# Performance work log

Hardware: AMD Instinct MI355X
Metric: run time of the kernel (lower is better)

## Reference

```python
import jax, jax.numpy as jnp
import numpy as np

COLOR_SIZE = 8
FILTERS = 64
LAYERS = 4
CUMSUM_NORM = 256 * 256 * 3  # hardcoded in original: /256/256/3


def setup_inputs() -> dict:
    key = jax.random.key(0)
    k0, k1, k2, k3 = jax.random.split(key, 4)
    s = 0.05
    example = jax.random.randint(k0, (4, 256, 256, 3), 0, COLOR_SIZE, dtype=jnp.int32)
    # per-channel Dense stacks: layer 0 has input dim 1, layers 1..3 have input dim FILTERS
    W_in_first = jax.random.normal(k1, (3, 1, FILTERS), dtype=jnp.float32) * s
    b_in_first = jnp.zeros((3, FILTERS), dtype=jnp.float32)
    W_in_rest = jax.random.normal(k2, (LAYERS - 1, 3, FILTERS, FILTERS), dtype=jnp.float32) * s
    b_in_rest = jnp.zeros((LAYERS - 1, 3, FILTERS), dtype=jnp.float32)
    W_final = jax.random.normal(k3, (3, FILTERS, COLOR_SIZE), dtype=jnp.float32) * s
    b_final = jnp.zeros((3, COLOR_SIZE), dtype=jnp.float32)
    return {
        "example": example,
        "W_in_first": W_in_first, "b_in_first": b_in_first,
        "W_in_rest": W_in_rest, "b_in_rest": b_in_rest,
        "W_final": W_final, "b_final": b_final,
    }


def reference(example, W_in_first, b_in_first, W_in_rest, b_in_rest, W_final, b_final):
    # example: [B, H, W, 3] int in [0, COLOR_SIZE)
    x = example.astype(jnp.float32) / COLOR_SIZE * 2.0 - 1.0
    B, H, W, _ = x.shape
    L = H * W
    x = x.reshape(B, L, 3, 1)

    def layer(x, Wl, bl):
        # per-channel dense + relu: [B, L, 3, din] x [3, din, dout] -> [B, L, 3, dout]
        x = jax.nn.relu(jnp.einsum('blcd,cde->blce', x, Wl) + bl)
        # flatten channels into the sequence and take causal running sum
        x = x.reshape(B, L * 3, FILTERS)
        x = jnp.cumsum(x, axis=-2) / CUMSUM_NORM
        return x.reshape(B, L, 3, FILTERS)

    x = layer(x, W_in_first, b_in_first)
    for i in range(LAYERS - 1):
        x = layer(x, W_in_rest[i], b_in_rest[i])

    # final per-channel dense to color logits (no activation)
    x = jnp.einsum('blcd,cde->blce', x, W_final) + b_final
    return x.reshape(B, H, W, 3, COLOR_SIZE)
```

## Files before the change

kernel.cpp:

```cpp
#include <hip/hip_runtime.h>
#include <stdint.h>


#define BB 4
#define SP 65536
#define SS 196608
#define CI 1024
#define NG 16
#define INVN (1.0f / 196608.0f)

typedef __attribute__((ext_vector_type(8))) _Float16 half8;
typedef __attribute__((ext_vector_type(4))) float    f32x4;

__global__ __launch_bounds__(256)
void prep(const int* __restrict__ ex, const float* __restrict__ W0,
          const float* __restrict__ b0, const float* __restrict__ Wr,
          const float* __restrict__ Wfin,
          _Float16* __restrict__ Wt16, _Float16* __restrict__ Wf16p,
          float* __restrict__ Wf32, float* __restrict__ tab32,
          int* __restrict__ Hsub, int* __restrict__ Hgrp)
{
    __shared__ int hist[64][24];
    int tid = threadIdx.x, bi = blockIdx.x;
    int b = bi >> 4, g = bi & 15;
    for (int i = tid; i < 1536; i += 256) hist[i / 24][i % 24] = 0;
    __syncthreads();
    for (int q = 0; q < 16; ++q) {
        int pl = q * 256 + tid;
        const int* ep = ex + ((size_t)b * SP + g * 4096 + pl) * 3;
        int j = pl >> 6;
        atomicAdd(&hist[j][ep[0]], 1);
        atomicAdd(&hist[j][8 + ep[1]], 1);
        atomicAdd(&hist[j][16 + ep[2]], 1);
    }
    __syncthreads();
    for (int i = tid; i < 1536; i += 256) {
        int j = i / 24, cv = i % 24;
        Hsub[(size_t)(b * CI + g * 64 + j) * 24 + cv] = hist[j][cv];
    }
    if (tid < 24) {
        int s = 0;
        for (int j = 0; j < 64; ++j) s += hist[j][tid];
        Hgrp[(size_t)(b * NG + g) * 24 + tid] = s;
    }
    {
        int i0 = bi * 256 + tid, nth = 64 * 256;
        for (int idx = i0; idx < 36864; idx += nth) {
            int d = idx & 63, f = (idx >> 6) & 63, lc = idx >> 12;
            Wt16[idx] = (_Float16)Wr[(size_t)(lc * 64 + d) * 64 + f];
        }
        for (int idx = i0; idx < 3072; idx += nth) {
            int d = idx & 63, n = (idx >> 6) & 15, c = idx >> 10;
            Wf16p[idx] = (n < 8) ? (_Float16)Wfin[(size_t)(c * 64 + d) * 8 + n]
                                 : (_Float16)0.f;
        }
        for (int idx = i0; idx < 1536; idx += nth) {
            int d = idx & 63, ck = idx >> 6;
            Wf32[idx] = Wfin[(size_t)((ck >> 3) * 64 + d) * 8 + (ck & 7)];
        }
        for (int idx = i0; idx < 1536; idx += nth) {
            int f = idx & 63, v = (idx >> 6) & 7, c = idx >> 9;
            float xv = v * 0.25f - 1.0f;
            tab32[idx] = fmaxf(W0[c * 64 + f] * xv + b0[c * 64 + f], 0.f);
        }
    }
}

__global__ __launch_bounds__(256, 4)
void midA(const int* __restrict__ ex,
          const int* __restrict__ Hsub, const int* __restrict__ Hgrp,
          const float* __restrict__ tab32,
          const _Float16* __restrict__ W16, const float* __restrict__ Wd32,
          const float* __restrict__ bias, _Float16* __restrict__ Y,
          float* __restrict__ A64, float* __restrict__ Ggrp)
{
    __shared__ float stab[1536];
    __shared__ __align__(16) _Float16 bounce3[3][64 * 72];
    __shared__ float segwt[3][4][64];
    __shared__ float basearr[192];
    __shared__ float hpart[4][24];
    __shared__ float carry[64];

    int tid = threadIdx.x, bi = blockIdx.x;
    int b = bi >> 10, ci = bi & 1023, g = ci >> 6, cr = ci & 63;
    int w = tid >> 6, ln = tid & 63, lm = ln & 15, lq = ln >> 4;
    int P0 = ci * 64;

    for (int i = tid; i < 1536; i += 256) stab[i] = tab32[i];
    if (ln < 24) {
        float s = 0.f;
        for (int j = w; j < g; j += 4)
            s += (float)Hgrp[(size_t)(b * NG + j) * 24 + ln];
        const int* hp = Hsub + (size_t)(b * CI + g * 64) * 24 + ln;
        for (int j = w; j < cr; j += 4) s += (float)hp[j * 24];
        hpart[w][ln] = s;
    }
    __syncthreads();

    float y0[3][16];
    {
#pragma unroll
        for (int p = 0; p < 16; ++p) {
            const int* ep = ex + ((size_t)b * SP + P0 + w * 16 + p) * 3;
            y0[0][p] = stab[ep[0] * 64 + ln];
            y0[1][p] = stab[(8 + ep[1]) * 64 + ln];
            y0[2][p] = stab[(16 + ep[2]) * 64 + ln];
        }
#pragma unroll
        for (int c = 0; c < 3; ++c)
#pragma unroll
            for (int p = 1; p < 16; ++p) y0[c][p] += y0[c][p - 1];
#pragma unroll
        for (int c = 0; c < 3; ++c) segwt[c][w][ln] = y0[c][15];
    }
    if (tid < 64) {
        float c0 = 0.f;
#pragma unroll
        for (int cv = 0; cv < 24; ++cv) {
            float cnt = hpart[0][cv] + hpart[1][cv] + hpart[2][cv] + hpart[3][cv];
            c0 += cnt * stab[cv * 64 + tid];
        }
        carry[tid] = c0;
    }
    __syncthreads();

    {
        float off0[3];
#pragma unroll
        for (int c = 0; c < 3; ++c) {
            float o = 0.f;
            for (int w2 = 0; w2 < w; ++w2) o += segwt[c][w2][ln];
            off0[c] = o;
        }
#pragma unroll
        for (int p = 0; p < 16; ++p) {
            float S0 = y0[0][p] + off0[0], S1 = y0[1][p] + off0[1], S2 = y0[2][p] + off0[2];
            float P1 = p ? y0[1][p - 1] + off0[1] : off0[1];
            float P2 = p ? y0[2][p - 1] + off0[2] : off0[2];
            int row = w * 16 + p;
            bounce3[0][row * 72 + ln] = (_Float16)(S0 + P1 + P2);
            bounce3[1][row * 72 + ln] = (_Float16)(S0 + S1 + P2);
            bounce3[2][row * 72 + ln] = (_Float16)(S0 + S1 + S2);
        }
    }
    if (tid < 192) {
        int c = tid >> 6, f = tid & 63;
        const float* wp = Wd32 + (size_t)(c * 64) * 64 + f;
        float a = 0.f;
        for (int d = 0; d < 64; ++d) a += carry[d] * wp[d * 64];
        basearr[tid] = bias[tid] + INVN * a;
    }
    __syncthreads();

    f32x4 acc[3][4];
#pragma unroll
    for (int c = 0; c < 3; ++c) {
        const half8* bb = (const half8*)&bounce3[c][0];
        half8 a0 = bb[(w * 16 + lm) * 9 + lq];
        half8 a1 = bb[(w * 16 + lm) * 9 + 4 + lq];
#pragma unroll
        for (int nt = 0; nt < 4; ++nt) {
            const half8* bp = (const half8*)(W16 + (size_t)(c * 64 + nt * 16 + lm) * 64);
            f32x4 t = {0.f, 0.f, 0.f, 0.f};
            t = __builtin_amdgcn_mfma_f32_16x16x32_f16(a0, bp[lq],     t, 0, 0, 0);
            t = __builtin_amdgcn_mfma_f32_16x16x32_f16(a1, bp[4 + lq], t, 0, 0, 0);
            acc[c][nt] = t;
        }
    }

    float s[3][4][4], wexcl[3][4];
#pragma unroll
    for (int c = 0; c < 3; ++c)
#pragma unroll
        for (int nt = 0; nt < 4; ++nt) {
            float base = basearr[c * 64 + nt * 16 + lm];
            float run = 0.f;
#pragma unroll
            for (int r = 0; r < 4; ++r) {
                float yv = fmaxf(base + INVN * acc[c][nt][r], 0.f);
                run += yv; s[c][nt][r] = run;
            }
            float v = run;
            float t1 = __shfl_up(v, 16); if (lq >= 1) v += t1;
            float t2 = __shfl_up(v, 32); if (lq >= 2) v += t2;
            wexcl[c][nt] = v - run;
            if (lq == 3) segwt[c][w][nt * 16 + lm] = v;
        }
    __syncthreads();

    {
        float off[3][4], tot[3][4];
#pragma unroll
        for (int c = 0; c < 3; ++c)
#pragma unroll
            for (int nt = 0; nt < 4; ++nt) {
                float o = wexcl[c][nt], ts = 0.f;
#pragma unroll
                for (int w2 = 0; w2 < 4; ++w2) {
                    float wv = segwt[c][w2][nt * 16 + lm];
                    ts += wv;
                    if (w2 < w) o += wv;
                }
                off[c][nt] = o; tot[c][nt] = ts;
            }
        if (w == 0 && lq == 0)
#pragma unroll
            for (int nt = 0; nt < 4; ++nt) {
                float t3 = tot[0][nt] + tot[1][nt] + tot[2][nt];
                A64[(size_t)(b * CI + ci) * 64 + nt * 16 + lm] = t3;
                atomicAdd(&Ggrp[(size_t)(b * NG + g) * 64 + nt * 16 + lm], t3);
            }
#pragma unroll
        for (int nt = 0; nt < 4; ++nt)
#pragma unroll
            for (int r = 0; r < 4; ++r) {
                float S0 = off[0][nt] + s[0][nt][r];
                float S1 = off[1][nt] + s[1][nt][r];
                float S2 = off[2][nt] + s[2][nt][r];
                float P1 = off[1][nt] + (r ? s[1][nt][r - 1] : 0.f);
                float P2 = off[2][nt] + (r ? s[2][nt][r - 1] : 0.f);
                int row = w * 16 + lq * 4 + r;
                bounce3[0][row * 72 + nt * 16 + lm] = (_Float16)(S0 + P1 + P2);
                bounce3[1][row * 72 + nt * 16 + lm] = (_Float16)(S0 + S1 + P2);
                bounce3[2][row * 72 + nt * 16 + lm] = (_Float16)(S0 + S1 + S2);
            }
    }
    __syncthreads();
#pragma unroll
    for (int q = 0; q < 6; ++q) {
        int idx = q * 256 + tid;
        int c = idx >> 9, rem = idx & 511;
        int pix = rem >> 3, f8 = rem & 7;
        half8 v = *(const half8*)&bounce3[c][pix * 72 + f8 * 8];
        ((half8*)(Y + ((size_t)(b * 3 + c) * SP + P0 + pix) * 64))[f8] = v;
    }
}

__global__ __launch_bounds__(256, 4)
void midB(const _Float16* Yin, _Float16* Yout,
          const float* __restrict__ A64p, const float* __restrict__ Ggrp_p,
          const _Float16* __restrict__ W16, const float* __restrict__ Wd32,
          const float* __restrict__ bias,
          float* __restrict__ A64, float* __restrict__ Ggrp)
{
    __shared__ __align__(16) _Float16 bounce3[3][64 * 72];
    __shared__ float wtop[3][4][64];
    __shared__ float basearr[192];
    __shared__ float cpart[4][64];
    __shared__ float carry[64];

    int tid = threadIdx.x, bi = blockIdx.x;
    int b = bi >> 10, ci = bi & 1023, g = ci >> 6, cr = ci & 63;
    int w = tid >> 6, ln = tid & 63, lm = ln & 15, lq = ln >> 4;
    int P0 = ci * 64;

    half8 af0[3], af1[3];
#pragma unroll
    for (int c = 0; c < 3; ++c) {
        const half8* ap = (const half8*)(Yin + ((size_t)(b * 3 + c) * SP + P0 + w * 16 + lm) * 64);
        af0[c] = ap[lq]; af1[c] = ap[4 + lq];
    }
    {
        float s = 0.f;
        for (int j = w; j < g; j += 4)
            s += Ggrp_p[(size_t)(b * NG + j) * 64 + ln];
        const float* ap = A64p + (size_t)(b * CI + g * 64) * 64 + ln;
        for (int j = w; j < cr; j += 4) s += ap[j * 64];
        cpart[w][ln] = s;
    }
    __syncthreads();
    if (tid < 64)
        carry[tid] = cpart[0][tid] + cpart[1][tid] + cpart[2][tid] + cpart[3][tid];
    __syncthreads();
    if (tid < 192) {
        int c = tid >> 6, f = tid & 63;
        const float* wp = Wd32 + (size_t)(c * 64) * 64 + f;
        float a = 0.f;
        for (int d = 0; d < 64; ++d) a += carry[d] * wp[d * 64];
        basearr[tid] = bias[tid] + INVN * a;
    }
    __syncthreads();

    f32x4 acc[3][4];
#pragma unroll
    for (int c = 0; c < 3; ++c)
#pragma unroll
        for (int nt = 0; nt < 4; ++nt) {
            const half8* bp = (const half8*)(W16 + (size_t)(c * 64 + nt * 16 + lm) * 64);
            f32x4 t = {0.f, 0.f, 0.f, 0.f};
            t = __builtin_amdgcn_mfma_f32_16x16x32_f16(af0[c], bp[lq],     t, 0, 0, 0);
            t = __builtin_amdgcn_mfma_f32_16x16x32_f16(af1[c], bp[4 + lq], t, 0, 0, 0);
            acc[c][nt] = t;
        }

    float s[3][4][4], wexcl[3][4];
#pragma unroll
    for (int c = 0; c < 3; ++c)
#pragma unroll
        for (int nt = 0; nt < 4; ++nt) {
            float base = basearr[c * 64 + nt * 16 + lm];
            float run = 0.f;
#pragma unroll
            for (int r = 0; r < 4; ++r) {
                float yv = fmaxf(base + INVN * acc[c][nt][r], 0.f);
                run += yv; s[c][nt][r] = run;
            }
            float v = run;
            float t1 = __shfl_up(v, 16); if (lq >= 1) v += t1;
            float t2 = __shfl_up(v, 32); if (lq >= 2) v += t2;
            wexcl[c][nt] = v - run;
            if (lq == 3) wtop[c][w][nt * 16 + lm] = v;
        }
    __syncthreads();

    {
        float off[3][4], tot[3][4];
#pragma unroll
        for (int c = 0; c < 3; ++c)
#pragma unroll
            for (int nt = 0; nt < 4; ++nt) {
                float o = wexcl[c][nt], ts = 0.f;
#pragma unroll
                for (int w2 = 0; w2 < 4; ++w2) {
                    float wv = wtop[c][w2][nt * 16 + lm];
                    ts += wv;
                    if (w2 < w) o += wv;
                }
                off[c][nt] = o; tot[c][nt] = ts;
            }
        if (w == 0 && lq == 0)
#pragma unroll
            for (int nt = 0; nt < 4; ++nt) {
                float t3 = tot[0][nt] + tot[1][nt] + tot[2][nt];
                A64[(size_t)(b * CI + ci) * 64 + nt * 16 + lm] = t3;
                atomicAdd(&Ggrp[(size_t)(b * NG + g) * 64 + nt * 16 + lm], t3);
            }
#pragma unroll
        for (int nt = 0; nt < 4; ++nt)
#pragma unroll
            for (int r = 0; r < 4; ++r) {
                float S0 = off[0][nt] + s[0][nt][r];
                float S1 = off[1][nt] + s[1][nt][r];
                float S2 = off[2][nt] + s[2][nt][r];
                float P1 = off[1][nt] + (r ? s[1][nt][r - 1] : 0.f);
                float P2 = off[2][nt] + (r ? s[2][nt][r - 1] : 0.f);
                int row = w * 16 + lq * 4 + r;
                bounce3[0][row * 72 + nt * 16 + lm] = (_Float16)(S0 + P1 + P2);
                bounce3[1][row * 72 + nt * 16 + lm] = (_Float16)(S0 + S1 + P2);
                bounce3[2][row * 72 + nt * 16 + lm] = (_Float16)(S0 + S1 + S2);
            }
    }
    __syncthreads();
#pragma unroll
    for (int q = 0; q < 6; ++q) {
        int idx = q * 256 + tid;
        int c = idx >> 9, rem = idx & 511;
        int pix = rem >> 3, f8 = rem & 7;
        half8 v = *(const half8*)&bounce3[c][pix * 72 + f8 * 8];
        ((half8*)(Yout + ((size_t)(b * 3 + c) * SP + P0 + pix) * 64))[f8] = v;
    }
}

__global__ __launch_bounds__(256, 4)
void midC(const _Float16* __restrict__ Yin,
          const float* __restrict__ A64p, const float* __restrict__ Ggrp_p,
          const _Float16* __restrict__ W16, const float* __restrict__ Wd32,
          const float* __restrict__ bias,
          const _Float16* __restrict__ Wf16p, const float* __restrict__ bfin,
          float* __restrict__ out, float* __restrict__ A64, float* __restrict__ Ggrp)
{
    __shared__ __align__(16) _Float16 bounce3[3][64 * 72];
    __shared__ float wtop[3][4][64];
    __shared__ float basearr[192];
    __shared__ float cpart[4][64];
    __shared__ float carry[64];
    __shared__ __align__(16) float outst[64 * 28];

    int tid = threadIdx.x, bi = blockIdx.x;
    int b = bi >> 10, ci = bi & 1023, g = ci >> 6, cr = ci & 63;
    int w = tid >> 6, ln = tid & 63, lm = ln & 15, lq = ln >> 4;
    int P0 = ci * 64;

    half8 af0[3], af1[3];
#pragma unroll
    for (int c = 0; c < 3; ++c) {
        const half8* ap = (const half8*)(Yin + ((size_t)(b * 3 + c) * SP + P0 + w * 16 + lm) * 64);
        af0[c] = ap[lq]; af1[c] = ap[4 + lq];
    }
    {
        float s = 0.f;
        for (int j = w; j < g; j += 4)
            s += Ggrp_p[(size_t)(b * NG + j) * 64 + ln];
        const float* ap = A64p + (size_t)(b * CI + g * 64) * 64 + ln;
        for (int j = w; j < cr; j += 4) s += ap[j * 64];
        cpart[w][ln] = s;
    }
    __syncthreads();
    if (tid < 64)
        carry[tid] = cpart[0][tid] + cpart[1][tid] + cpart[2][tid] + cpart[3][tid];
    __syncthreads();
    if (tid < 192) {
        int c = tid >> 6, f = tid & 63;
        const float* wp = Wd32 + (size_t)(c * 64) * 64 + f;
        float a = 0.f;
        for (int d = 0; d < 64; ++d) a += carry[d] * wp[d * 64];
        basearr[tid] = bias[tid] + INVN * a;
    }
    __syncthreads();

    f32x4 acc[3][4];
#pragma unroll
    for (int c = 0; c < 3; ++c)
#pragma unroll
        for (int nt = 0; nt < 4; ++nt) {
            const half8* bp = (const half8*)(W16 + (size_t)(c * 64 + nt * 16 + lm) * 64);
            f32x4 t = {0.f, 0.f, 0.f, 0.f};
            t = __builtin_amdgcn_mfma_f32_16x16x32_f16(af0[c], bp[lq],     t, 0, 0, 0);
            t = __builtin_amdgcn_mfma_f32_16x16x32_f16(af1[c], bp[4 + lq], t, 0, 0, 0);
            acc[c][nt] = t;
        }

    float s[3][4][4], wexcl[3][4];
#pragma unroll
    for (int c = 0; c < 3; ++c)
#pragma unroll
        for (int nt = 0; nt < 4; ++nt) {
            float base = basearr[c * 64 + nt * 16 + lm];
            float run = 0.f;
#pragma unroll
            for (int r = 0; r < 4; ++r) {
                float yv = fmaxf(base + INVN * acc[c][nt][r], 0.f);
                run += yv; s[c][nt][r] = run;
            }
            float v = run;
            float t1 = __shfl_up(v, 16); if (lq >= 1) v += t1;
            float t2 = __shfl_up(v, 32); if (lq >= 2) v += t2;
            wexcl[c][nt] = v - run;
            if (lq == 3) wtop[c][w][nt * 16 + lm] = v;
        }
    __syncthreads();

    {
        float off[3][4], tot[3][4];
#pragma unroll
        for (int c = 0; c < 3; ++c)
#pragma unroll
            for (int nt = 0; nt < 4; ++nt) {
                float o = wexcl[c][nt], ts = 0.f;
#pragma unroll
                for (int w2 = 0; w2 < 4; ++w2) {
                    float wv = wtop[c][w2][nt * 16 + lm];
                    ts += wv;
                    if (w2 < w) o += wv;
                }
                off[c][nt] = o; tot[c][nt] = ts;
            }
        if (w == 0 && lq == 0)
#pragma unroll
            for (int nt = 0; nt < 4; ++nt) {
                float t3 = tot[0][nt] + tot[1][nt] + tot[2][nt];
                A64[(size_t)(b * CI + ci) * 64 + nt * 16 + lm] = t3;
                atomicAdd(&Ggrp[(size_t)(b * NG + g) * 64 + nt * 16 + lm], t3);
            }
#pragma unroll
        for (int nt = 0; nt < 4; ++nt)
#pragma unroll
            for (int r = 0; r < 4; ++r) {
                float S0 = off[0][nt] + s[0][nt][r];
                float S1 = off[1][nt] + s[1][nt][r];
                float S2 = off[2][nt] + s[2][nt][r];
                float P1 = off[1][nt] + (r ? s[1][nt][r - 1] : 0.f);
                float P2 = off[2][nt] + (r ? s[2][nt][r - 1] : 0.f);
                int row = w * 16 + lq * 4 + r;
                bounce3[0][row * 72 + nt * 16 + lm] = (_Float16)(S0 + P1 + P2);
                bounce3[1][row * 72 + nt * 16 + lm] = (_Float16)(S0 + S1 + P2);
                bounce3[2][row * 72 + nt * 16 + lm] = (_Float16)(S0 + S1 + S2);
            }
    }
    __syncthreads();

#pragma unroll
    for (int c = 0; c < 3; ++c) {
        const half8* bb = (const half8*)&bounce3[c][0];
        half8 fa0 = bb[(w * 16 + lm) * 9 + lq];
        half8 fa1 = bb[(w * 16 + lm) * 9 + 4 + lq];
        const half8* fb = (const half8*)(Wf16p + (size_t)(c * 16 + lm) * 64);
        f32x4 t = {0.f, 0.f, 0.f, 0.f};
        t = __builtin_amdgcn_mfma_f32_16x16x32_f16(fa0, fb[lq],     t, 0, 0, 0);
        t = __builtin_amdgcn_mfma_f32_16x16x32_f16(fa1, fb[4 + lq], t, 0, 0, 0);
        if (lm < 8) {
            float bz = bfin[c * 8 + lm];
#pragma unroll
            for (int r = 0; r < 4; ++r)
                outst[(w * 16 + lq * 4 + r) * 28 + c * 8 + lm] = bz + INVN * t[r];
        }
    }
    __syncthreads();
    {
        float4* obase = (float4*)(out + ((size_t)b * SS + (size_t)P0 * 3) * 8);
#pragma unroll
        for (int k = 0; k < 2; ++k) {
            int idx = k * 256 + tid;
            if (idx < 384) {
                int pix = idx / 6, sub = (idx % 6) * 4;
                obase[idx] = *(const float4*)&outst[pix * 28 + sub];
            }
        }
    }
}

__global__ __launch_bounds__(256, 4)
void fixk(const float* __restrict__ A64p, const float* __restrict__ Ggrp_p,
          const float* __restrict__ Wf32, float* __restrict__ out)
{
    __shared__ float cpart[4][64];
    __shared__ float carry[64];
    __shared__ float vfix[24];
    int tid = threadIdx.x, bi = blockIdx.x;
    int b = bi >> 10, ci = bi & 1023, g = ci >> 6, cr = ci & 63;
    int w = tid >> 6, ln = tid & 63;
    int P0 = ci * 64;

    {
        float s = 0.f;
        for (int j = w; j < g; j += 4)
            s += Ggrp_p[(size_t)(b * NG + j) * 64 + ln];
        const float* ap = A64p + (size_t)(b * CI + g * 64) * 64 + ln;
        for (int j = w; j < cr; j += 4) s += ap[j * 64];
        cpart[w][ln] = s;
    }
    __syncthreads();
    if (tid < 64)
        carry[tid] = cpart[0][tid] + cpart[1][tid] + cpart[2][tid] + cpart[3][tid];
    __syncthreads();
    if (tid < 24) {
        float vf = 0.f;
        for (int d = 0; d < 64; ++d) vf += carry[d] * Wf32[tid * 64 + d];
        vfix[tid] = INVN * vf;
    }
    __syncthreads();
    float4* obase = (float4*)(out + ((size_t)b * SS + (size_t)P0 * 3) * 8);
#pragma unroll
    for (int k = 0; k < 2; ++k) {
        int idx = k * 256 + tid;
        if (idx < 384) {
            int sub = (idx % 6) * 4;
            float4 v = obase[idx];
            v.x += vfix[sub];
            v.y += vfix[sub + 1];
            v.z += vfix[sub + 2];
            v.w += vfix[sub + 3];
            obase[idx] = v;
        }
    }
}

extern "C" void kernel_launch(void* const* d_in, const int* in_sizes, int n_in,
                              void* d_out, int out_size, void* d_ws, size_t ws_size,
                              hipStream_t stream)
{
    const int*   ex   = (const int*)d_in[0];
    const float* W0   = (const float*)d_in[1];
    const float* b0   = (const float*)d_in[2];
    const float* Wr   = (const float*)d_in[3];
    const float* br   = (const float*)d_in[4];
    const float* Wfin = (const float*)d_in[5];
    const float* bfin = (const float*)d_in[6];
    float* out = (float*)d_out;

    char* ws = (char*)d_ws;
    size_t off = 0;
    _Float16* Y = (_Float16*)(ws + off); off += (size_t)BB * 3 * SP * 64 * 2;
    float* Ggrp1 = (float*)(ws + off); off += (size_t)BB * NG * 64 * 4;
    float* Ggrp2 = (float*)(ws + off); off += (size_t)BB * NG * 64 * 4;
    float* Ggrp3 = (float*)(ws + off); off += (size_t)BB * NG * 64 * 4;
    float* A64_1 = (float*)(ws + off); off += (size_t)BB * CI * 64 * 4;
    float* A64_2 = (float*)(ws + off); off += (size_t)BB * CI * 64 * 4;
    float* A64_3 = (float*)(ws + off); off += (size_t)BB * CI * 64 * 4;
    int* Hsub = (int*)(ws + off); off += (size_t)BB * CI * 24 * 4;
    int* Hgrp = (int*)(ws + off); off += (size_t)BB * NG * 24 * 4;
    _Float16* Wt16  = (_Float16*)(ws + off); off += 36864 * 2;
    _Float16* Wf16p = (_Float16*)(ws + off); off += 3072 * 2;
    float* Wf32  = (float*)(ws + off); off += 1536 * 4;
    float* tab32 = (float*)(ws + off); off += 1536 * 4;

    hipMemsetAsync(Ggrp1, 0, 3 * (size_t)BB * NG * 64 * 4, stream);
    prep<<<64, 256, 0, stream>>>(ex, W0, b0, Wr, Wfin,
                                 Wt16, Wf16p, Wf32, tab32, Hsub, Hgrp);
    midA<<<4096, 256, 0, stream>>>(ex, Hsub, Hgrp, tab32,
                                   Wt16, Wr, br, Y, A64_1, Ggrp1);
    midB<<<4096, 256, 0, stream>>>(Y, Y, A64_1, Ggrp1,
                                   Wt16 + 12288, Wr + 12288, br + 192,
                                   A64_2, Ggrp2);
    midC<<<4096, 256, 0, stream>>>(Y, A64_2, Ggrp2,
                                   Wt16 + 24576, Wr + 24576, br + 384,
                                   Wf16p, bfin, out, A64_3, Ggrp3);
    fixk<<<4096, 256, 0, stream>>>(A64_3, Ggrp3, Wf32, out);
}
```

Baseline: 365.2 us.

## Shrink LDS staging buffers, raise occupancy, widen prep grid, parallelize fix reduction

```diff
diff --git a/kernel.cpp b/kernel.cpp
--- a/kernel.cpp
+++ b/kernel.cpp
@@ -20,31 +20,31 @@
           float* __restrict__ Wf32, float* __restrict__ tab32,
           int* __restrict__ Hsub, int* __restrict__ Hgrp)
 {
-    __shared__ int hist[64][24];
+    __shared__ int hist[16][24];
     int tid = threadIdx.x, bi = blockIdx.x;
-    int b = bi >> 4, g = bi & 15;
-    for (int i = tid; i < 1536; i += 256) hist[i / 24][i % 24] = 0;
-    __syncthreads();
-    for (int q = 0; q < 16; ++q) {
-        int pl = q * 256 + tid;
-        const int* ep = ex + ((size_t)b * SP + g * 4096 + pl) * 3;
+    int b = bi >> 6, g = (bi >> 2) & 15, q = bi & 3;
+    for (int i = tid; i < 384; i += 256) hist[i / 24][i % 24] = 0;
+    __syncthreads();
+    for (int it = 0; it < 4; ++it) {
+        int pl = it * 256 + tid;
+        const int* ep = ex + ((size_t)b * SP + g * 4096 + q * 1024 + pl) * 3;
         int j = pl >> 6;
         atomicAdd(&hist[j][ep[0]], 1);
         atomicAdd(&hist[j][8 + ep[1]], 1);
         atomicAdd(&hist[j][16 + ep[2]], 1);
     }
     __syncthreads();
-    for (int i = tid; i < 1536; i += 256) {
+    for (int i = tid; i < 384; i += 256) {
         int j = i / 24, cv = i % 24;
-        Hsub[(size_t)(b * CI + g * 64 + j) * 24 + cv] = hist[j][cv];
+        Hsub[(size_t)(b * CI + g * 64 + q * 16 + j) * 24 + cv] = hist[j][cv];
     }
     if (tid < 24) {
         int s = 0;
-        for (int j = 0; j < 64; ++j) s += hist[j][tid];
-        Hgrp[(size_t)(b * NG + g) * 24 + tid] = s;
-    }
-    {
-        int i0 = bi * 256 + tid, nth = 64 * 256;
+        for (int j = 0; j < 16; ++j) s += hist[j][tid];
+        atomicAdd(&Hgrp[(size_t)(b * NG + g) * 24 + tid], s);
+    }
+    {
+        int i0 = bi * 256 + tid, nth = 256 * 256;
         for (int idx = i0; idx < 36864; idx += nth) {
             int d = idx & 63, f = (idx >> 6) & 63, lc = idx >> 12;
             Wt16[idx] = (_Float16)Wr[(size_t)(lc * 64 + d) * 64 + f];
@@ -66,7 +66,7 @@
     }
 }
 
-__global__ __launch_bounds__(256, 4)
+__global__ __launch_bounds__(256, 6)
 void midA(const int* __restrict__ ex,
           const int* __restrict__ Hsub, const int* __restrict__ Hgrp,
           const float* __restrict__ tab32,
@@ -75,7 +75,7 @@
           float* __restrict__ A64, float* __restrict__ Ggrp)
 {
     __shared__ float stab[1536];
-    __shared__ __align__(16) _Float16 bounce3[3][64 * 72];
+    __shared__ __align__(16) _Float16 bounce[64 * 72];
     __shared__ float segwt[3][4][64];
     __shared__ float basearr[192];
     __shared__ float hpart[4][24];
@@ -124,24 +124,12 @@
     }
     __syncthreads();
 
-    {
-        float off0[3];
-#pragma unroll
-        for (int c = 0; c < 3; ++c) {
-            float o = 0.f;
-            for (int w2 = 0; w2 < w; ++w2) o += segwt[c][w2][ln];
-            off0[c] = o;
-        }
-#pragma unroll
-        for (int p = 0; p < 16; ++p) {
-            float S0 = y0[0][p] + off0[0], S1 = y0[1][p] + off0[1], S2 = y0[2][p] + off0[2];
-            float P1 = p ? y0[1][p - 1] + off0[1] : off0[1];
-            float P2 = p ? y0[2][p - 1] + off0[2] : off0[2];
-            int row = w * 16 + p;
-            bounce3[0][row * 72 + ln] = (_Float16)(S0 + P1 + P2);
-            bounce3[1][row * 72 + ln] = (_Float16)(S0 + S1 + P2);
-            bounce3[2][row * 72 + ln] = (_Float16)(S0 + S1 + S2);
-        }
+    float off0[3];
+#pragma unroll
+    for (int c = 0; c < 3; ++c) {
+        float o = 0.f;
+        for (int w2 = 0; w2 < w; ++w2) o += segwt[c][w2][ln];
+        off0[c] = o;
     }
     if (tid < 192) {
         int c = tid >> 6, f = tid & 63;
@@ -150,23 +138,35 @@
         for (int d = 0; d < 64; ++d) a += carry[d] * wp[d * 64];
         basearr[tid] = bias[tid] + INVN * a;
     }
-    __syncthreads();
+
+    half8 af0[3], af1[3];
+#pragma unroll
+    for (int c = 0; c < 3; ++c) {
+#pragma unroll
+        for (int p = 0; p < 16; ++p) {
+            float a0 = y0[0][p] + off0[0];
+            float a1 = (c >= 1 ? y0[1][p] : (p ? y0[1][p - 1] : 0.f)) + off0[1];
+            float a2 = (c == 2 ? y0[2][p] : (p ? y0[2][p - 1] : 0.f)) + off0[2];
+            bounce[(w * 16 + p) * 72 + ln] = (_Float16)(a0 + a1 + a2);
+        }
+        __syncthreads();
+        const half8* bb = (const half8*)bounce;
+        af0[c] = bb[(w * 16 + lm) * 9 + lq];
+        af1[c] = bb[(w * 16 + lm) * 9 + 4 + lq];
+        __syncthreads();
+    }
 
     f32x4 acc[3][4];
 #pragma unroll
-    for (int c = 0; c < 3; ++c) {
-        const half8* bb = (const half8*)&bounce3[c][0];
-        half8 a0 = bb[(w * 16 + lm) * 9 + lq];
-        half8 a1 = bb[(w * 16 + lm) * 9 + 4 + lq];
+    for (int c = 0; c < 3; ++c)
 #pragma unroll
         for (int nt = 0; nt < 4; ++nt) {
             const half8* bp = (const half8*)(W16 + (size_t)(c * 64 + nt * 16 + lm) * 64);
             f32x4 t = {0.f, 0.f, 0.f, 0.f};
-            t = __builtin_amdgcn_mfma_f32_16x16x32_f16(a0, bp[lq],     t, 0, 0, 0);
-            t = __builtin_amdgcn_mfma_f32_16x16x32_f16(a1, bp[4 + lq], t, 0, 0, 0);
+            t = __builtin_amdgcn_mfma_f32_16x16x32_f16(af0[c], bp[lq],     t, 0, 0, 0);
+            t = __builtin_amdgcn_mfma_f32_16x16x32_f16(af1[c], bp[4 + lq], t, 0, 0, 0);
             acc[c][nt] = t;
         }
-    }
 
     float s[3][4][4], wexcl[3][4];
 #pragma unroll
@@ -210,40 +210,33 @@
                 A64[(size_t)(b * CI + ci) * 64 + nt * 16 + lm] = t3;
                 atomicAdd(&Ggrp[(size_t)(b * NG + g) * 64 + nt * 16 + lm], t3);
             }
-#pragma unroll
-        for (int nt = 0; nt < 4; ++nt)
+        _Float16* Y0 = Y + ((size_t)(b * 3) * SP + P0 + w * 16 + lq * 4) * 64 + lm;
+        _Float16* Y1 = Y0 + (size_t)SP * 64;
+        _Float16* Y2 = Y1 + (size_t)SP * 64;
+#pragma unroll
+        for (int nt = 0; nt < 4; ++nt) {
+            float offT = off[0][nt] + off[1][nt] + off[2][nt];
 #pragma unroll
             for (int r = 0; r < 4; ++r) {
-                float S0 = off[0][nt] + s[0][nt][r];
-                float S1 = off[1][nt] + s[1][nt][r];
-                float S2 = off[2][nt] + s[2][nt][r];
-                float P1 = off[1][nt] + (r ? s[1][nt][r - 1] : 0.f);
-                float P2 = off[2][nt] + (r ? s[2][nt][r - 1] : 0.f);
-                int row = w * 16 + lq * 4 + r;
-                bounce3[0][row * 72 + nt * 16 + lm] = (_Float16)(S0 + P1 + P2);
-                bounce3[1][row * 72 + nt * 16 + lm] = (_Float16)(S0 + S1 + P2);
-                bounce3[2][row * 72 + nt * 16 + lm] = (_Float16)(S0 + S1 + S2);
-            }
-    }
-    __syncthreads();
-#pragma unroll
-    for (int q = 0; q < 6; ++q) {
-        int idx = q * 256 + tid;
-        int c = idx >> 9, rem = idx & 511;
-        int pix = rem >> 3, f8 = rem & 7;
-        half8 v = *(const half8*)&bounce3[c][pix * 72 + f8 * 8];
-        ((half8*)(Y + ((size_t)(b * 3 + c) * SP + P0 + pix) * 64))[f8] = v;
+                float s1p = r ? s[1][nt][r - 1] : 0.f;
+                float s2p = r ? s[2][nt][r - 1] : 0.f;
+                float V  = offT + s[0][nt][r];
+                float Wv = V + s[1][nt][r];
+                Y0[r * 64 + nt * 16] = (_Float16)(V + s1p + s2p);
+                Y1[r * 64 + nt * 16] = (_Float16)(Wv + s2p);
+                Y2[r * 64 + nt * 16] = (_Float16)(Wv + s[2][nt][r]);
+            }
+        }
     }
 }
 
-__global__ __launch_bounds__(256, 4)
+__global__ __launch_bounds__(256, 8)
 void midB(const _Float16* Yin, _Float16* Yout,
           const float* __restrict__ A64p, const float* __restrict__ Ggrp_p,
           const _Float16* __restrict__ W16, const float* __restrict__ Wd32,
           const float* __restrict__ bias,
           float* __restrict__ A64, float* __restrict__ Ggrp)
 {
-    __shared__ __align__(16) _Float16 bounce3[3][64 * 72];
     __shared__ float wtop[3][4][64];
     __shared__ float basearr[192];
     __shared__ float cpart[4][64];
@@ -268,6 +261,18 @@
         for (int j = w; j < cr; j += 4) s += ap[j * 64];
         cpart[w][ln] = s;
     }
+
+    f32x4 acc[3][4];
+#pragma unroll
+    for (int c = 0; c < 3; ++c)
+#pragma unroll
+        for (int nt = 0; nt < 4; ++nt) {
+            const half8* bp = (const half8*)(W16 + (size_t)(c * 64 + nt * 16 + lm) * 64);
+            f32x4 t = {0.f, 0.f, 0.f, 0.f};
+            t = __builtin_amdgcn_mfma_f32_16x16x32_f16(af0[c], bp[lq],     t, 0, 0, 0);
+            t = __builtin_amdgcn_mfma_f32_16x16x32_f16(af1[c], bp[4 + lq], t, 0, 0, 0);
+            acc[c][nt] = t;
+        }
     __syncthreads();
     if (tid < 64)
         carry[tid] = cpart[0][tid] + cpart[1][tid] + cpart[2][tid] + cpart[3][tid];
@@ -281,18 +286,6 @@
     }
     __syncthreads();
 
-    f32x4 acc[3][4];
-#pragma unroll
-    for (int c = 0; c < 3; ++c)
-#pragma unroll
-        for (int nt = 0; nt < 4; ++nt) {
-            const half8* bp = (const half8*)(W16 + (size_t)(c * 64 + nt * 16 + lm) * 64);
-            f32x4 t = {0.f, 0.f, 0.f, 0.f};
-            t = __builtin_amdgcn_mfma_f32_16x16x32_f16(af0[c], bp[lq],     t, 0, 0, 0);
-            t = __builtin_amdgcn_mfma_f32_16x16x32_f16(af1[c], bp[4 + lq], t, 0, 0, 0);
-            acc[c][nt] = t;
-        }
-
     float s[3][4][4], wexcl[3][4];
 #pragma unroll
     for (int c = 0; c < 3; ++c)
@@ -335,33 +328,27 @@
                 A64[(size_t)(b * CI + ci) * 64 + nt * 16 + lm] = t3;
                 atomicAdd(&Ggrp[(size_t)(b * NG + g) * 64 + nt * 16 + lm], t3);
             }
-#pragma unroll
-        for (int nt = 0; nt < 4; ++nt)
+        _Float16* Y0 = Yout + ((size_t)(b * 3) * SP + P0 + w * 16 + lq * 4) * 64 + lm;
+        _Float16* Y1 = Y0 + (size_t)SP * 64;
+        _Float16* Y2 = Y1 + (size_t)SP * 64;
+#pragma unroll
+        for (int nt = 0; nt < 4; ++nt) {
+            float offT = off[0][nt] + off[1][nt] + off[2][nt];
 #pragma unroll
             for (int r = 0; r < 4; ++r) {
-                float S0 = off[0][nt] + s[0][nt][r];
-                float S1 = off[1][nt] + s[1][nt][r];
-                float S2 = off[2][nt] + s[2][nt][r];
-                float P1 = off[1][nt] + (r ? s[1][nt][r - 1] : 0.f);
-                float P2 = off[2][nt] + (r ? s[2][nt][r - 1] : 0.f);
-                int row = w * 16 + lq * 4 + r;
-                bounce3[0][row * 72 + nt * 16 + lm] = (_Float16)(S0 + P1 + P2);
-                bounce3[1][row * 72 + nt * 16 + lm] = (_Float16)(S0 + S1 + P2);
-                bounce3[2][row * 72 + nt * 16 + lm] = (_Float16)(S0 + S1 + S2);
-            }
-    }
-    __syncthreads();
-#pragma unroll
-    for (int q = 0; q < 6; ++q) {
-        int idx = q * 256 + tid;
-        int c = idx >> 9, rem = idx & 511;
-        int pix = rem >> 3, f8 = rem & 7;
-        half8 v = *(const half8*)&bounce3[c][pix * 72 + f8 * 8];
-        ((half8*)(Yout + ((size_t)(b * 3 + c) * SP + P0 + pix) * 64))[f8] = v;
+                float s1p = r ? s[1][nt][r - 1] : 0.f;
+                float s2p = r ? s[2][nt][r - 1] : 0.f;
+                float V  = offT + s[0][nt][r];
+                float Wv = V + s[1][nt][r];
+                Y0[r * 64 + nt * 16] = (_Float16)(V + s1p + s2p);
+                Y1[r * 64 + nt * 16] = (_Float16)(Wv + s2p);
+                Y2[r * 64 + nt * 16] = (_Float16)(Wv + s[2][nt][r]);
+            }
+        }
     }
 }
 
-__global__ __launch_bounds__(256, 4)
+__global__ __launch_bounds__(256, 6)
 void midC(const _Float16* __restrict__ Yin,
           const float* __restrict__ A64p, const float* __restrict__ Ggrp_p,
           const _Float16* __restrict__ W16, const float* __restrict__ Wd32,
@@ -369,12 +356,11 @@
           const _Float16* __restrict__ Wf16p, const float* __restrict__ bfin,
           float* __restrict__ out, float* __restrict__ A64, float* __restrict__ Ggrp)
 {
-    __shared__ __align__(16) _Float16 bounce3[3][64 * 72];
+    __shared__ __align__(16) _Float16 bounce[64 * 72];
     __shared__ float wtop[3][4][64];
     __shared__ float basearr[192];
     __shared__ float cpart[4][64];
     __shared__ float carry[64];
-    __shared__ __align__(16) float outst[64 * 28];
 
     int tid = threadIdx.x, bi = blockIdx.x;
     int b = bi >> 10, ci = bi & 1023, g = ci >> 6, cr = ci & 63;
@@ -395,6 +381,18 @@
         for (int j = w; j < cr; j += 4) s += ap[j * 64];
         cpart[w][ln] = s;
     }
+
+    f32x4 acc[3][4];
+#pragma unroll
+    for (int c = 0; c < 3; ++c)
+#pragma unroll
+        for (int nt = 0; nt < 4; ++nt) {
+            const half8* bp = (const half8*)(W16 + (size_t)(c * 64 + nt * 16 + lm) * 64);
+            f32x4 t = {0.f, 0.f, 0.f, 0.f};
+            t = __builtin_amdgcn_mfma_f32_16x16x32_f16(af0[c], bp[lq],     t, 0, 0, 0);
+            t = __builtin_amdgcn_mfma_f32_16x16x32_f16(af1[c], bp[4 + lq], t, 0, 0, 0);
+            acc[c][nt] = t;
+        }
     __syncthreads();
     if (tid < 64)
         carry[tid] = cpart[0][tid] + cpart[1][tid] + cpart[2][tid] + cpart[3][tid];
@@ -408,18 +406,6 @@
     }
     __syncthreads();
 
-    f32x4 acc[3][4];
-#pragma unroll
-    for (int c = 0; c < 3; ++c)
-#pragma unroll
-        for (int nt = 0; nt < 4; ++nt) {
-            const half8* bp = (const half8*)(W16 + (size_t)(c * 64 + nt * 16 + lm) * 64);
-            f32x4 t = {0.f, 0.f, 0.f, 0.f};
-            t = __builtin_amdgcn_mfma_f32_16x16x32_f16(af0[c], bp[lq],     t, 0, 0, 0);
-            t = __builtin_amdgcn_mfma_f32_16x16x32_f16(af1[c], bp[4 + lq], t, 0, 0, 0);
-            acc[c][nt] = t;
-        }
-
     float s[3][4][4], wexcl[3][4];
 #pragma unroll
     for (int c = 0; c < 3; ++c)
@@ -440,8 +426,9 @@
         }
     __syncthreads();
 
-    {
-        float off[3][4], tot[3][4];
+    float off[3][4];
+    {
+        float tot[3][4];
 #pragma unroll
         for (int c = 0; c < 3; ++c)
 #pragma unroll
@@ -462,26 +449,27 @@
                 A64[(size_t)(b * CI + ci) * 64 + nt * 16 + lm] = t3;
                 atomicAdd(&Ggrp[(size_t)(b * NG + g) * 64 + nt * 16 + lm], t3);
             }
-#pragma unroll
-        for (int nt = 0; nt < 4; ++nt)
+    }
+
+#pragma unroll
+    for (int c = 0; c < 3; ++c) {
+#pragma unroll
+        for (int nt = 0; nt < 4; ++nt) {
+            float offT = off[0][nt] + off[1][nt] + off[2][nt];
 #pragma unroll
             for (int r = 0; r < 4; ++r) {
-                float S0 = off[0][nt] + s[0][nt][r];
-                float S1 = off[1][nt] + s[1][nt][r];
-                float S2 = off[2][nt] + s[2][nt][r];
-                float P1 = off[1][nt] + (r ? s[1][nt][r - 1] : 0.f);
-                float P2 = off[2][nt] + (r ? s[2][nt][r - 1] : 0.f);
-                int row = w * 16 + lq * 4 + r;
-                bounce3[0][row * 72 + nt * 16 + lm] = (_Float16)(S0 + P1 + P2);
-                bounce3[1][row * 72 + nt * 16 + lm] = (_Float16)(S0 + S1 + P2);
-                bounce3[2][row * 72 + nt * 16 + lm] = (_Float16)(S0 + S1 + S2);
-            }
-    }
-    __syncthreads();
-
-#pragma unroll
-    for (int c = 0; c < 3; ++c) {
-        const half8* bb = (const half8*)&bounce3[c][0];
+                float s1p = r ? s[1][nt][r - 1] : 0.f;
+                float s2p = r ? s[2][nt][r - 1] : 0.f;
+                float V = offT + s[0][nt][r];
+                float ov;
+                if (c == 0)      ov = V + s1p + s2p;
+                else if (c == 1) ov = V + s[1][nt][r] + s2p;
+                else             ov = V + s[1][nt][r] + s[2][nt][r];
+                bounce[(w * 16 + lq * 4 + r) * 72 + nt * 16 + lm] = (_Float16)ov;
+            }
+        }
+        __syncthreads();
+        const half8* bb = (const half8*)bounce;
         half8 fa0 = bb[(w * 16 + lm) * 9 + lq];
         half8 fa1 = bb[(w * 16 + lm) * 9 + 4 + lq];
         const half8* fb = (const half8*)(Wf16p + (size_t)(c * 16 + lm) * 64);
@@ -490,31 +478,22 @@
         t = __builtin_amdgcn_mfma_f32_16x16x32_f16(fa1, fb[4 + lq], t, 0, 0, 0);
         if (lm < 8) {
             float bz = bfin[c * 8 + lm];
+            float* ob = out + ((size_t)b * SS + (size_t)(P0 + w * 16 + lq * 4) * 3 + c) * 8 + lm;
 #pragma unroll
             for (int r = 0; r < 4; ++r)
-                outst[(w * 16 + lq * 4 + r) * 28 + c * 8 + lm] = bz + INVN * t[r];
-        }
-    }
-    __syncthreads();
-    {
-        float4* obase = (float4*)(out + ((size_t)b * SS + (size_t)P0 * 3) * 8);
-#pragma unroll
-        for (int k = 0; k < 2; ++k) {
-            int idx = k * 256 + tid;
-            if (idx < 384) {
-                int pix = idx / 6, sub = (idx % 6) * 4;
-                obase[idx] = *(const float4*)&outst[pix * 28 + sub];
-            }
-        }
+                ob[r * 24] = bz + INVN * t[r];
+        }
+        __syncthreads();
     }
 }
 
-__global__ __launch_bounds__(256, 4)
+__global__ __launch_bounds__(256, 8)
 void fixk(const float* __restrict__ A64p, const float* __restrict__ Ggrp_p,
           const float* __restrict__ Wf32, float* __restrict__ out)
 {
     __shared__ float cpart[4][64];
     __shared__ float carry[64];
+    __shared__ float part[24][8];
     __shared__ float vfix[24];
     int tid = threadIdx.x, bi = blockIdx.x;
     int b = bi >> 10, ci = bi & 1023, g = ci >> 6, cr = ci & 63;
@@ -533,9 +512,20 @@
     if (tid < 64)
         carry[tid] = cpart[0][tid] + cpart[1][tid] + cpart[2][tid] + cpart[3][tid];
     __syncthreads();
+    if (tid < 192) {
+        int ck = tid >> 3, sg = tid & 7;
+        const float* wp = Wf32 + ck * 64 + sg * 8;
+        const float* cp = carry + sg * 8;
+        float vf = 0.f;
+#pragma unroll
+        for (int d = 0; d < 8; ++d) vf += cp[d] * wp[d];
+        part[ck][sg] = vf;
+    }
+    __syncthreads();
     if (tid < 24) {
         float vf = 0.f;
-        for (int d = 0; d < 64; ++d) vf += carry[d] * Wf32[tid * 64 + d];
+#pragma unroll
+        for (int j = 0; j < 8; ++j) vf += part[tid][j];
         vfix[tid] = INVN * vf;
     }
     __syncthreads();
@@ -585,8 +575,9 @@
     float* tab32 = (float*)(ws + off); off += 1536 * 4;
 
     hipMemsetAsync(Ggrp1, 0, 3 * (size_t)BB * NG * 64 * 4, stream);
-    prep<<<64, 256, 0, stream>>>(ex, W0, b0, Wr, Wfin,
-                                 Wt16, Wf16p, Wf32, tab32, Hsub, Hgrp);
+    hipMemsetAsync(Hgrp, 0, (size_t)BB * NG * 24 * 4, stream);
+    prep<<<256, 256, 0, stream>>>(ex, W0, b0, Wr, Wfin,
+                                  Wt16, Wf16p, Wf32, tab32, Hsub, Hgrp);
     midA<<<4096, 256, 0, stream>>>(ex, Hsub, Hgrp, tab32,
                                    Wt16, Wr, br, Y, A64_1, Ggrp1);
     midB<<<4096, 256, 0, stream>>>(Y, Y, A64_1, Ggrp1,
```

New measurement: 591.9 us. 62.1% more time.
